# Optimization experiments

Measured on AMD Instinct MI355X. Metric: run time of the kernel, lower is better.

The kernel has to match this reference:

```python
import jax, jax.numpy as jnp
import numpy as np

B, T, PAST, HID = 2, 512, 4096, 4096
HQ, HKV, D = 32, 8, 128
HH_SIZE, RECENT = 512, 512
CACHE = HH_SIZE + RECENT
MAX_POS = PAST + T


def rotate_half(x):
    h = x.shape[-1] // 2
    return jnp.concatenate([-x[..., h:], x[..., :h]], axis=-1)


def setup_inputs() -> dict:
    key = jax.random.key(0)
    ks = jax.random.split(key, 9)
    hidden_states = jax.random.normal(ks[0], (B, T, HID), jnp.float32) * 0.02
    past_k = jax.random.normal(ks[1], (B, HKV, PAST, D), jnp.float32)
    past_v = jax.random.normal(ks[2], (B, HKV, PAST, D), jnp.float32)
    # accumulated heavy-hitter scores are nonnegative attention-mass sums
    hh_prev = jax.random.uniform(ks[3], (B, HKV, PAST), jnp.float32) * float(T)
    wq = jax.random.normal(ks[4], (HID, HQ * D), jnp.float32) * 0.02
    wk = jax.random.normal(ks[5], (HID, HKV * D), jnp.float32) * 0.02
    wv = jax.random.normal(ks[6], (HID, HKV * D), jnp.float32) * 0.02
    wo = jax.random.normal(ks[7], (HQ * D, HID), jnp.float32) * 0.02
    # RoPE tables [1, MAX_POS, D]
    inv_freq = 1.0 / (10000.0 ** (jnp.arange(0, D, 2, dtype=jnp.float32) / D))
    t = jnp.arange(MAX_POS, dtype=jnp.float32)
    freqs = jnp.einsum('t,f->tf', t, inv_freq)
    emb = jnp.concatenate([freqs, freqs], axis=-1)
    cos = jnp.cos(emb)[None]
    sin = jnp.sin(emb)[None]
    position_ids = jnp.broadcast_to(PAST + jnp.arange(T, dtype=jnp.int32)[None, :], (B, T))
    return {"hidden_states": hidden_states, "past_k": past_k, "past_v": past_v,
            "hh_prev": hh_prev, "wq": wq, "wk": wk, "wv": wv, "wo": wo,
            "cos": cos, "sin": sin, "position_ids": position_ids}


def reference(hidden_states, past_k, past_v, hh_prev, wq, wk, wv, wo, cos, sin, position_ids):
    b, t, _ = hidden_states.shape
    # projections -> [B, H, T, D]
    q = (hidden_states @ wq).reshape(b, t, HQ, D).transpose(0, 2, 1, 3)
    k_new = (hidden_states @ wk).reshape(b, t, HKV, D).transpose(0, 2, 1, 3)
    v_new = (hidden_states @ wv).reshape(b, t, HKV, D).transpose(0, 2, 1, 3)
    # RoPE: gather cos/sin at position_ids -> [B, 1, T, D]
    cos_g = cos[0][position_ids][:, None]
    sin_g = sin[0][position_ids][:, None]
    q = q * cos_g + rotate_half(q) * sin_g
    k_new = k_new * cos_g + rotate_half(k_new) * sin_g
    k = jnp.concatenate([past_k, k_new], axis=2)   # [B, HKV, S, D]
    v = jnp.concatenate([past_v, v_new], axis=2)
    s = k.shape[2]
    past_len = s - t
    g = HQ // HKV
    k_rep = jnp.repeat(k, g, axis=1)               # repeat_interleave over heads
    v_rep = jnp.repeat(v, g, axis=1)
    scores = jnp.einsum('bhtd,bhsd->bhts', q, k_rep) / jnp.sqrt(jnp.float32(D))
    causal = jnp.arange(s)[None, :] <= (past_len + jnp.arange(t))[:, None]  # [T, S]
    scores = jnp.where(causal[None, None], scores, jnp.finfo(scores.dtype).min)
    attn = jax.nn.softmax(scores, axis=-1)         # [B, HQ, T, S]
    ctx = jnp.einsum('bhts,bhsd->bhtd', attn, v_rep)
    out = ctx.transpose(0, 2, 1, 3).reshape(b, t, HQ * D) @ wo
    # --- H2O heavy-hitter score update ('average' GQA reduction) ---
    sc = attn.sum(axis=2)                          # [B, HQ, S]
    sc = sc.reshape(b, HKV, g, s).mean(axis=2)     # [B, HKV, S]
    hh = sc.at[:, :, :past_len].add(hh_prev)
    # --- eviction: topk heavy hitters outside recent window + recent window ---
    select = hh[:, :, : s - RECENT]
    _, top = jax.lax.top_k(select, HH_SIZE)
    top = jnp.sort(top, axis=-1)
    recent_idx = jnp.broadcast_to(jnp.arange(s - RECENT, s, dtype=top.dtype), (b, HKV, RECENT))
    keep = jnp.concatenate([top, recent_idx], axis=-1)      # [B, HKV, CACHE]
    k_kept = jnp.take_along_axis(k, keep[..., None], axis=2)
    v_kept = jnp.take_along_axis(v, keep[..., None], axis=2)
    hh_new = jnp.take_along_axis(hh, keep, axis=2)
    return out, k_kept, v_kept, hh_new
```

## Files before the change

### kernel.cpp

```cpp
#include <hip/hip_runtime.h>
#include <cstdint>
#include <cstddef>

typedef unsigned short u16;
typedef __attribute__((ext_vector_type(8))) short short8;
typedef __attribute__((ext_vector_type(4))) float floatx4;

static __device__ __forceinline__ u16 f2bf(float f){
  union { float f; uint32_t i; } u; u.f = f;
  uint32_t i = u.i;
  return (u16)((i + 0x7FFFu + ((i >> 16) & 1u)) >> 16);
}

struct __align__(8) U16x4 { u16 a,b,c,d; };

__global__ void k_convert(const float* __restrict__ src, u16* __restrict__ dst, int n4){
  int i = blockIdx.x*256 + threadIdx.x;
  if (i >= n4) return;
  float4 v = ((const float4*)src)[i];
  U16x4 o{f2bf(v.x), f2bf(v.y), f2bf(v.z), f2bf(v.w)};
  ((U16x4*)dst)[i] = o;
}

__global__ void k_copy_pastk(const float* __restrict__ pk, u16* __restrict__ kcat){
  int i = blockIdx.x*256 + threadIdx.x;
  int slice = i >> 17;
  int off   = i & 131071;
  float4 v = ((const float4*)pk)[i];
  U16x4 o{f2bf(v.x), f2bf(v.y), f2bf(v.z), f2bf(v.w)};
  ((U16x4*)(kcat + (size_t)slice*(4608*128)))[off] = o;
}

__global__ void k_transpose(const float* __restrict__ src, u16* __restrict__ dst,
                            int lds_, int ldd, size_t sstride, size_t dstride){
  src += (size_t)blockIdx.z * sstride; dst += (size_t)blockIdx.z * dstride;
  __shared__ float tile[32][33];
  int bm = blockIdx.y*32, bn = blockIdx.x*32;
  int tx = threadIdx.x & 31, ty = threadIdx.x >> 5;
  #pragma unroll
  for (int r = 0; r < 32; r += 8)
    tile[r+ty][tx] = src[(size_t)(bm + r + ty)*lds_ + bn + tx];
  __syncthreads();
  #pragma unroll
  for (int r = 0; r < 32; r += 8)
    dst[(size_t)(bn + r + ty)*ldd + bm + tx] = f2bf(tile[tx][r+ty]);
}

__global__ __launch_bounds__(256) void k_gemm_bt(
    const u16* __restrict__ A, const u16* __restrict__ Bt, float* __restrict__ C,
    int N, int K)
{
  __shared__ __align__(16) u16 As[128*64];
  __shared__ __align__(16) u16 Bs[128*64];
  const int tid = threadIdx.x, lane = tid & 63, wave = tid >> 6;
  const int m0 = blockIdx.y*128, n0 = blockIdx.x*128;
  const int wr = (wave >> 1)*64, wc = (wave & 1)*64;
  const int srow = tid >> 3, sc8 = tid & 7;
  const u16* ap = A  + (size_t)(m0 + srow)*K + sc8*8;
  const u16* bp = Bt + (size_t)(n0 + srow)*K + sc8*8;
  floatx4 acc[4][4] = {};
  short8 ra[4], rb[4];
  #pragma unroll
  for (int i = 0; i < 4; ++i){
    ra[i] = *(const short8*)(ap + (size_t)i*32*K);
    rb[i] = *(const short8*)(bp + (size_t)i*32*K);
  }
  const int nk = K >> 6;
  for (int kt = 0; kt < nk; ++kt){
    #pragma unroll
    for (int i = 0; i < 4; ++i){
      const int r = srow + i*32;
      const int c = sc8 ^ (r & 7);
      *(short8*)(As + r*64 + c*8) = ra[i];
      *(short8*)(Bs + r*64 + c*8) = rb[i];
    }
    __syncthreads();
    if (kt + 1 < nk){
      const size_t ko = (size_t)(kt+1)*64;
      #pragma unroll
      for (int i = 0; i < 4; ++i){
        ra[i] = *(const short8*)(ap + (size_t)i*32*K + ko);
        rb[i] = *(const short8*)(bp + (size_t)i*32*K + ko);
      }
    }
    #pragma unroll
    for (int ks = 0; ks < 2; ++ks){
      const int c16 = ks*4 + (lane >> 4);
      short8 af[4], bf[4];
      #pragma unroll
      for (int mi = 0; mi < 4; ++mi){
        const int r = wr + mi*16 + (lane & 15);
        af[mi] = *(const short8*)(As + r*64 + ((c16 ^ (r & 7))*8));
      }
      #pragma unroll
      for (int ni = 0; ni < 4; ++ni){
        const int r = wc + ni*16 + (lane & 15);
        bf[ni] = *(const short8*)(Bs + r*64 + ((c16 ^ (r & 7))*8));
      }
      #pragma unroll
      for (int mi = 0; mi < 4; ++mi)
        #pragma unroll
        for (int ni = 0; ni < 4; ++ni)
          acc[mi][ni] = __builtin_amdgcn_mfma_f32_16x16x32_bf16(af[mi], bf[ni], acc[mi][ni], 0,0,0);
    }
    __syncthreads();
  }
  #pragma unroll
  for (int mi = 0; mi < 4; ++mi)
    #pragma unroll
    for (int ni = 0; ni < 4; ++ni){
      const int col = n0 + wc + ni*16 + (lane & 15);
      const int row = m0 + wr + mi*16 + ((lane >> 4) << 2);
      #pragma unroll
      for (int j = 0; j < 4; ++j)
        C[(size_t)(row + j)*N + col] = acc[mi][ni][j];
    }
}

__global__ void k_rope_q(const float* __restrict__ qf, const float* __restrict__ cosb,
                         const float* __restrict__ sinb, const int* __restrict__ pid,
                         u16* __restrict__ qbo){
  int gid = blockIdx.x*256 + threadIdx.x;
  int d = gid & 63, hh = (gid >> 6) & 31, m = gid >> 11;
  int b = m >> 9, t = m & 511;
  int p = pid[b*512 + t];
  float c = cosb[(size_t)p*128 + d], s = sinb[(size_t)p*128 + d];
  size_t ib = (size_t)m*4096 + hh*128 + d;
  float x = qf[ib], y = qf[ib + 64];
  const float sc = 0.08838834764831845f;
  size_t ob = (((size_t)(b*32 + hh))*512 + t)*128 + d;
  qbo[ob]      = f2bf((x*c - y*s)*sc);
  qbo[ob + 64] = f2bf((y*c + x*s)*sc);
}

__global__ void k_rope_kv(const float* __restrict__ kvf, const float* __restrict__ cosb,
                          const float* __restrict__ sinb, const int* __restrict__ pid,
                          u16* __restrict__ kcat, float* __restrict__ knr, u16* __restrict__ vtcat){
  int gid = blockIdx.x*256 + threadIdx.x;
  int d = gid & 63, kv = (gid >> 6) & 7, m = gid >> 9;
  int b = m >> 9, t = m & 511;
  int p = pid[b*512 + t];
  float c = cosb[(size_t)p*128 + d], s = sinb[(size_t)p*128 + d];
  size_t ib = (size_t)m*2048 + kv*128 + d;
  float x = kvf[ib], y = kvf[ib + 64];
  float k0 = x*c - y*s, k1 = y*c + x*s;
  int bk = b*8 + kv;
  size_t kb = ((size_t)bk*4608 + 4096 + t)*128 + d;
  kcat[kb] = f2bf(k0); kcat[kb + 64] = f2bf(k1);
  size_t nb = ((size_t)bk*512 + t)*128 + d;
  knr[nb] = k0; knr[nb + 64] = k1;
  float v0 = kvf[ib + 1024], v1 = kvf[ib + 1088];
  size_t vb = (size_t)bk*(128*4608) + (size_t)d*4608 + 4096 + t;
  vtcat[vb] = f2bf(v0);
  vtcat[vb + (size_t)64*4608] = f2bf(v1);
}

__global__ __launch_bounds__(256) void k_attn(
    const u16* __restrict__ qb, const u16* __restrict__ kcat,
    const u16* __restrict__ vtcat, u16* __restrict__ ctxb,
    float* __restrict__ part_sc)
{
  __shared__ __align__(16) u16 kvlds[64*128];
  __shared__ __align__(16) float plds[64*68];
  __shared__ float cs[4608];

  const int tid = threadIdx.x, lane = tid & 63, wave = tid >> 6;
  const int bid = blockIdx.x;
  const int slice  = (bid & 7) + 8*((bid >> 3) >> 5);
  const int within = (bid >> 3) & 31;
  const int b  = slice >> 3;
  const int kv = slice & 7;
  const int h  = kv*4 + (within >> 3);
  const int tb = within & 7;
  const int t0 = tb * 64;

  const u16* qp = qb + (((size_t)(b*32 + h))*512 + t0) * 128;
  const u16* kp = kcat  + (size_t)slice * (4608*128);
  const u16* vp = vtcat + (size_t)slice * (128*4608);

  for (int i = tid; i < 4608; i += 256) cs[i] = 0.f;

  short8 qf[4];
  {
    const int r = wave*16 + (lane & 15);
    const u16* q0 = qp + (size_t)r*128 + ((lane>>4)*8);
    #pragma unroll
    for (int ks = 0; ks < 4; ++ks) qf[ks] = *(const short8*)(q0 + ks*32);
  }

  const int ntiles = 65 + tb;
  float l0=0.f, l1=0.f, l2=0.f, l3=0.f;

  for (int st = 0; st < ntiles; ++st){
    const int s0 = st * 64;
    __syncthreads();
    {
      const int c16 = tid & 15;
      #pragma unroll
      for (int i = 0; i < 4; ++i){
        const int row = i*16 + (tid >> 4);
        short8 v = *(const short8*)(kp + (size_t)(s0 + row)*128 + c16*8);
        *(short8*)(kvlds + row*128 + ((c16 ^ (row & 7))*8)) = v;
      }
    }
    __syncthreads();
    floatx4 sacc[4] = {};
    #pragma unroll
    for (int ks = 0; ks < 4; ++ks){
      const int c16 = ks*4 + (lane >> 4);
      #pragma unroll
      for (int nf = 0; nf < 4; ++nf){
        const int r = nf*16 + (lane & 15);
        short8 kf = *(const short8*)(kvlds + r*128 + ((c16 ^ (r & 7))*8));
        sacc[nf] = __builtin_amdgcn_mfma_f32_16x16x32_bf16(qf[ks], kf, sacc[nf], 0,0,0);
      }
    }
    const bool lastt = (st == ntiles-1);
    #pragma unroll
    for (int nf = 0; nf < 4; ++nf){
      #pragma unroll
      for (int j = 0; j < 4; ++j){
        float e = __expf(sacc[nf][j]);
        if (lastt){
          int scol = nf*16 + (lane & 15);
          int tloc = wave*16 + ((lane >> 4) << 2) + j;
          if (scol > tloc) e = 0.f;
        }
        if (j==0) l0 += e; else if (j==1) l1 += e; else if (j==2) l2 += e; else l3 += e;
      }
    }
  }
  #pragma unroll
  for (int m = 1; m <= 8; m <<= 1){
    l0 += __shfl_xor(l0, m); l1 += __shfl_xor(l1, m);
    l2 += __shfl_xor(l2, m); l3 += __shfl_xor(l3, m);
  }
  const float rl0 = 1.f/l0, rl1 = 1.f/l1, rl2 = 1.f/l2, rl3 = 1.f/l3;

  floatx4 pacc[8] = {};
  const int prow = wave*16 + (lane & 15);
  for (int st = 0; st < ntiles; ++st){
    const int s0 = st*64;
    __syncthreads();
    {
      const int c16 = tid & 15;
      #pragma unroll
      for (int i = 0; i < 4; ++i){
        const int row = i*16 + (tid >> 4);
        short8 v = *(const short8*)(kp + (size_t)(s0 + row)*128 + c16*8);
        *(short8*)(kvlds + row*128 + ((c16 ^ (row & 7))*8)) = v;
      }
    }
    __syncthreads();
    floatx4 sacc[4] = {};
    #pragma unroll
    for (int ks = 0; ks < 4; ++ks){
      const int c16 = ks*4 + (lane >> 4);
      #pragma unroll
      for (int nf = 0; nf < 4; ++nf){
        const int r = nf*16 + (lane & 15);
        short8 kf = *(const short8*)(kvlds + r*128 + ((c16 ^ (r & 7))*8));
        sacc[nf] = __builtin_amdgcn_mfma_f32_16x16x32_bf16(qf[ks], kf, sacc[nf], 0,0,0);
      }
    }
    const bool lastt = (st == ntiles-1);
    float cs0=0.f, cs1=0.f, cs2=0.f, cs3=0.f;
    #pragma unroll
    for (int nf = 0; nf < 4; ++nf){
      float cpart = 0.f;
      #pragma unroll
      for (int j = 0; j < 4; ++j){
        float e = __expf(sacc[nf][j]);
        if (lastt){
          int scol = nf*16 + (lane & 15);
          int tloc = wave*16 + ((lane >> 4) << 2) + j;
          if (scol > tloc) e = 0.f;
        }
        float rl = (j==0)?rl0:(j==1)?rl1:(j==2)?rl2:rl3;
        float p = e * rl;
        plds[(wave*16 + ((lane>>4)<<2) + j)*68 + nf*16 + (lane & 15)] = p;
        cpart += p;
      }
      if (nf==0) cs0=cpart; else if (nf==1) cs1=cpart; else if (nf==2) cs2=cpart; else cs3=cpart;
    }
    cs0 += __shfl_xor(cs0,16); cs0 += __shfl_xor(cs0,32);
    cs1 += __shfl_xor(cs1,16); cs1 += __shfl_xor(cs1,32);
    cs2 += __shfl_xor(cs2,16); cs2 += __shfl_xor(cs2,32);
    cs3 += __shfl_xor(cs3,16); cs3 += __shfl_xor(cs3,32);
    {
      const int nfsel = lane >> 4;
      float v = (nfsel==0)?cs0:(nfsel==1)?cs1:(nfsel==2)?cs2:cs3;
      atomicAdd(&cs[s0 + nfsel*16 + (lane & 15)], v);
    }
    __syncthreads();
    {
      const int c = tid & 7;
      #pragma unroll
      for (int i = 0; i < 4; ++i){
        const int row = i*32 + (tid >> 3);
        short8 v = *(const short8*)(vp + (size_t)row*4608 + s0 + c*8);
        *(short8*)(kvlds + row*64 + ((c ^ (row & 7))*8)) = v;
      }
    }
    __syncthreads();
    short8 pa[2];
    #pragma unroll
    for (int k2 = 0; k2 < 2; ++k2){
      const int sbase = k2*32 + ((lane>>4)*8);
      const float* pp = plds + prow*68 + sbase;
      float4 x = *(const float4*)pp;
      float4 y = *(const float4*)(pp + 4);
      short8 t8;
      t8[0]=(short)f2bf(x.x); t8[1]=(short)f2bf(x.y); t8[2]=(short)f2bf(x.z); t8[3]=(short)f2bf(x.w);
      t8[4]=(short)f2bf(y.x); t8[5]=(short)f2bf(y.y); t8[6]=(short)f2bf(y.z); t8[7]=(short)f2bf(y.w);
      pa[k2] = t8;
    }
    #pragma unroll
    for (int nf = 0; nf < 8; ++nf){
      const int rv = nf*16 + (lane & 15);
      #pragma unroll
      for (int k2 = 0; k2 < 2; ++k2){
        const int c = ((k2*4 + (lane>>4)) ^ (rv & 7));
        short8 vf = *(const short8*)(kvlds + rv*64 + c*8);
        pacc[nf] = __builtin_amdgcn_mfma_f32_16x16x32_bf16(pa[k2], vf, pacc[nf], 0,0,0);
      }
    }
  }
  #pragma unroll
  for (int nf = 0; nf < 8; ++nf)
    #pragma unroll
    for (int j = 0; j < 4; ++j){
      const int trow = t0 + wave*16 + ((lane>>4)<<2) + j;
      const int col  = h*128 + nf*16 + (lane & 15);
      ctxb[(size_t)(b*512 + trow)*4096 + col] = f2bf(pacc[nf][j]);
    }
  __syncthreads();
  {
    float* pr = part_sc + (((size_t)(b*32 + h))*8 + tb)*4608;
    for (int i = tid; i < 4608; i += 256) pr[i] = cs[i];
  }
}

__global__ void k_hh_reduce(const float* __restrict__ part, const float* __restrict__ hhprev,
                            float* __restrict__ hh){
  int gid = blockIdx.x*256 + threadIdx.x;
  if (gid >= 73728) return;
  int s = gid % 4608; int bk = gid / 4608; int b = bk >> 3, kv = bk & 7;
  float acc = 0.f;
  #pragma unroll
  for (int h4 = 0; h4 < 4; ++h4){
    const float* pp = part + (((size_t)(b*32 + kv*4 + h4))*8)*4608 + s;
    #pragma unroll
    for (int tbb = 0; tbb < 8; ++tbb) acc += pp[(size_t)tbb*4608];
  }
  acc *= 0.25f;
  if (s < 4096) acc += hhprev[(size_t)bk*4096 + s];
  hh[gid] = acc;
}

__global__ __launch_bounds__(256) void k_topk(const float* __restrict__ hh, int* __restrict__ keep,
                                              float* __restrict__ hh_new){
  __shared__ uint64_t keys[4096];
  __shared__ int sidx[512];
  const int bk = blockIdx.x, tid = threadIdx.x;
  const float* hp = hh + (size_t)bk*4608;
  for (int i = tid; i < 4096; i += 256){
    uint32_t vb = __float_as_uint(hp[i]);
    keys[i] = ((uint64_t)(0xFFFFFFFFu - vb) << 12) | (uint32_t)i;
  }
  __syncthreads();
  for (int k = 2; k <= 4096; k <<= 1){
    for (int j = k >> 1; j > 0; j >>= 1){
      for (int i = tid; i < 4096; i += 256){
        int ixj = i ^ j;
        if (ixj > i){
          uint64_t a = keys[i], c = keys[ixj];
          bool up = ((i & k) == 0);
          if ((a > c) == up){ keys[i] = c; keys[ixj] = a; }
        }
      }
      __syncthreads();
    }
  }
  for (int i = tid; i < 512; i += 256) sidx[i] = (int)(keys[i] & 0xFFF);
  __syncthreads();
  for (int k = 2; k <= 512; k <<= 1){
    for (int j = k >> 1; j > 0; j >>= 1){
      for (int i = tid; i < 512; i += 256){
        int ixj = i ^ j;
        if (ixj > i){
          int a = sidx[i], c = sidx[ixj];
          bool up = ((i & k) == 0);
          if ((a > c) == up){ sidx[i] = c; sidx[ixj] = a; }
        }
      }
      __syncthreads();
    }
  }
  for (int i = tid; i < 512; i += 256){
    int id = sidx[i];
    keep[bk*1024 + i] = id;
    hh_new[(size_t)bk*1024 + i] = hp[id];
    keep[bk*1024 + 512 + i] = 4096 + i;
    hh_new[(size_t)bk*1024 + 512 + i] = hp[4096 + i];
  }
}

__global__ void k_gather(const float* __restrict__ pastk, const float* __restrict__ pastv,
                         const float* __restrict__ knr, const float* __restrict__ kvf,
                         const int* __restrict__ keep,
                         float* __restrict__ outk, float* __restrict__ outv){
  int r = blockIdx.x*2 + (threadIdx.x >> 7);
  int lane = threadIdx.x & 127;
  int bk = r >> 10, i = r & 1023;
  int idx = keep[bk*1024 + i];
  float kval, vval;
  if (idx < 4096){
    kval = pastk[((size_t)bk*4096 + idx)*128 + lane];
    vval = pastv[((size_t)bk*4096 + idx)*128 + lane];
  } else {
    int t = idx - 4096; int b = bk >> 3, kv = bk & 7;
    kval = knr[((size_t)bk*512 + t)*128 + lane];
    vval = kvf[(size_t)(b*512 + t)*2048 + 1024 + kv*128 + lane];
  }
  outk[(size_t)r*128 + lane] = kval;
  outv[(size_t)r*128 + lane] = vval;
}

extern "C" void kernel_launch(void* const* d_in, const int* in_sizes, int n_in,
                              void* d_out, int out_size, void* d_ws, size_t ws_size,
                              hipStream_t stream){
  const float* hs     = (const float*)d_in[0];
  const float* pastk  = (const float*)d_in[1];
  const float* pastv  = (const float*)d_in[2];
  const float* hhprev = (const float*)d_in[3];
  const float* wq     = (const float*)d_in[4];
  const float* wk     = (const float*)d_in[5];
  const float* wv     = (const float*)d_in[6];
  const float* wo     = (const float*)d_in[7];
  const float* cosb   = (const float*)d_in[8];
  const float* sinb   = (const float*)d_in[9];
  const int*   pid    = (const int*)d_in[10];
  float* out = (float*)d_out;
  char* ws = (char*)d_ws;

  u16*   hsb  = (u16*)(ws + 0);
  u16*   wqt  = (u16*)(ws + 8388608);
  u16*   wkvt = (u16*)(ws + 41943040);
  float* qf   = (float*)(ws + 58720256);
  float* part = qf;
  float* kvf  = (float*)(ws + 75497472);
  u16*   qb   = (u16*)(ws + 83886080);
  u16*   kcat = (u16*)(ws + 92274688);
  u16*   vtc  = (u16*)(ws + 111149056);
  float* knr  = (float*)(ws + 130023424);
  u16*   ctxb = (u16*)(ws + 138412032);
  float* hhb  = (float*)(ws + 146800640);
  int*   keep = (int*)(ws + 147095552);

  (void)in_sizes; (void)n_in; (void)out_size; (void)ws_size;

  k_convert<<<4096,256,0,stream>>>(hs, hsb, 1048576);
  k_transpose<<<dim3(128,128,1),256,0,stream>>>(wq, wqt, 4096, 4096, 0, 0);
  k_transpose<<<dim3(32,128,1),256,0,stream>>>(wk, wkvt, 1024, 4096, 0, 0);
  k_transpose<<<dim3(32,128,1),256,0,stream>>>(wv, wkvt + (size_t)1024*4096, 1024, 4096, 0, 0);
  k_transpose<<<dim3(4,128,16),256,0,stream>>>(pastv, vtc, 128, 4608,
                                               (size_t)4096*128, (size_t)128*4608);
  k_copy_pastk<<<8192,256,0,stream>>>(pastk, kcat);

  k_gemm_bt<<<dim3(32,8),256,0,stream>>>(hsb, wqt, qf, 4096, 4096);
  k_gemm_bt<<<dim3(16,8),256,0,stream>>>(hsb, wkvt, kvf, 2048, 4096);
  k_transpose<<<dim3(128,128,1),256,0,stream>>>(wo, wqt, 4096, 4096, 0, 0);

  k_rope_q<<<8192,256,0,stream>>>(qf, cosb, sinb, pid, qb);
  k_rope_kv<<<2048,256,0,stream>>>(kvf, cosb, sinb, pid, kcat, knr, vtc);

  k_attn<<<512,256,0,stream>>>(qb, kcat, vtc, ctxb, part);

  k_gemm_bt<<<dim3(32,8),256,0,stream>>>(ctxb, wqt, out, 4096, 4096);

  k_hh_reduce<<<288,256,0,stream>>>(part, hhprev, hhb);
  k_topk<<<16,256,0,stream>>>(hhb, keep, out + 8388608);
  k_gather<<<8192,256,0,stream>>>(pastk, pastv, knr, kvf, keep,
                                  out + 4194304, out + 6291456);
}
```

Before: 906.5 us.

## Split-K GEMMs and split attention into parallel row-sum and PV passes

Adds split-K (two K halves written to separate buffers) to the projection and output GEMMs, so each launches twice as many blocks; the halves are summed in the rope kernels and a new add kernel. Attention is split into a row-sum-of-exp pass over 2048 blocks, each covering a chunk of key tiles, followed by a PV pass with register-prefetched K and V tiles loaded together. Column sums go to a per-wave LDS buffer and are written directly instead of through shared atomics. The gather recomputes RoPE for new keys instead of storing a float copy. The cost is more memory traffic for partial buffers and an extra QK pass.

Result: faster. 789.3 us (-12.9%).

```diff
diff --git a/kernel.cpp b/kernel.cpp
--- a/kernel.cpp
+++ b/kernel.cpp
@@ -48,24 +48,26 @@
 
 __global__ __launch_bounds__(256) void k_gemm_bt(
     const u16* __restrict__ A, const u16* __restrict__ Bt, float* __restrict__ C,
-    int N, int K)
+    int N, int Kfull, int kLen, size_t cstride)
 {
   __shared__ __align__(16) u16 As[128*64];
   __shared__ __align__(16) u16 Bs[128*64];
   const int tid = threadIdx.x, lane = tid & 63, wave = tid >> 6;
   const int m0 = blockIdx.y*128, n0 = blockIdx.x*128;
+  const int kOff = blockIdx.z * kLen;
+  C += (size_t)blockIdx.z * cstride;
   const int wr = (wave >> 1)*64, wc = (wave & 1)*64;
   const int srow = tid >> 3, sc8 = tid & 7;
-  const u16* ap = A  + (size_t)(m0 + srow)*K + sc8*8;
-  const u16* bp = Bt + (size_t)(n0 + srow)*K + sc8*8;
+  const u16* ap = A  + (size_t)(m0 + srow)*Kfull + kOff + sc8*8;
+  const u16* bp = Bt + (size_t)(n0 + srow)*Kfull + kOff + sc8*8;
   floatx4 acc[4][4] = {};
   short8 ra[4], rb[4];
   #pragma unroll
   for (int i = 0; i < 4; ++i){
-    ra[i] = *(const short8*)(ap + (size_t)i*32*K);
-    rb[i] = *(const short8*)(bp + (size_t)i*32*K);
-  }
-  const int nk = K >> 6;
+    ra[i] = *(const short8*)(ap + (size_t)i*32*Kfull);
+    rb[i] = *(const short8*)(bp + (size_t)i*32*Kfull);
+  }
+  const int nk = kLen >> 6;
   for (int kt = 0; kt < nk; ++kt){
     #pragma unroll
     for (int i = 0; i < 4; ++i){
@@ -79,8 +81,8 @@
       const size_t ko = (size_t)(kt+1)*64;
       #pragma unroll
       for (int i = 0; i < 4; ++i){
-        ra[i] = *(const short8*)(ap + (size_t)i*32*K + ko);
-        rb[i] = *(const short8*)(bp + (size_t)i*32*K + ko);
+        ra[i] = *(const short8*)(ap + (size_t)i*32*Kfull + ko);
+        rb[i] = *(const short8*)(bp + (size_t)i*32*Kfull + ko);
       }
     }
     #pragma unroll
@@ -117,171 +119,238 @@
     }
 }
 
-__global__ void k_rope_q(const float* __restrict__ qf, const float* __restrict__ cosb,
-                         const float* __restrict__ sinb, const int* __restrict__ pid,
-                         u16* __restrict__ qbo){
+__global__ void k_add(const float* __restrict__ a, const float* __restrict__ b,
+                      float* __restrict__ o, int n4){
+  int i = blockIdx.x*256 + threadIdx.x;
+  if (i >= n4) return;
+  float4 x = ((const float4*)a)[i], y = ((const float4*)b)[i];
+  float4 z; z.x=x.x+y.x; z.y=x.y+y.y; z.z=x.z+y.z; z.w=x.w+y.w;
+  ((float4*)o)[i] = z;
+}
+
+__global__ void k_rope_q(const float* __restrict__ qfA, const float* __restrict__ qfB,
+                         const float* __restrict__ cosb, const float* __restrict__ sinb,
+                         const int* __restrict__ pid, u16* __restrict__ qbo){
   int gid = blockIdx.x*256 + threadIdx.x;
   int d = gid & 63, hh = (gid >> 6) & 31, m = gid >> 11;
   int b = m >> 9, t = m & 511;
   int p = pid[b*512 + t];
   float c = cosb[(size_t)p*128 + d], s = sinb[(size_t)p*128 + d];
   size_t ib = (size_t)m*4096 + hh*128 + d;
-  float x = qf[ib], y = qf[ib + 64];
+  float x = qfA[ib] + qfB[ib], y = qfA[ib+64] + qfB[ib+64];
   const float sc = 0.08838834764831845f;
   size_t ob = (((size_t)(b*32 + hh))*512 + t)*128 + d;
   qbo[ob]      = f2bf((x*c - y*s)*sc);
   qbo[ob + 64] = f2bf((y*c + x*s)*sc);
 }
 
-__global__ void k_rope_kv(const float* __restrict__ kvf, const float* __restrict__ cosb,
-                          const float* __restrict__ sinb, const int* __restrict__ pid,
-                          u16* __restrict__ kcat, float* __restrict__ knr, u16* __restrict__ vtcat){
+__global__ void k_rope_kv(const float* __restrict__ kvfA, const float* __restrict__ kvfB,
+                          const float* __restrict__ cosb, const float* __restrict__ sinb,
+                          const int* __restrict__ pid,
+                          u16* __restrict__ kcat, u16* __restrict__ vtcat){
   int gid = blockIdx.x*256 + threadIdx.x;
   int d = gid & 63, kv = (gid >> 6) & 7, m = gid >> 9;
   int b = m >> 9, t = m & 511;
   int p = pid[b*512 + t];
   float c = cosb[(size_t)p*128 + d], s = sinb[(size_t)p*128 + d];
   size_t ib = (size_t)m*2048 + kv*128 + d;
-  float x = kvf[ib], y = kvf[ib + 64];
+  float x = kvfA[ib] + kvfB[ib], y = kvfA[ib+64] + kvfB[ib+64];
   float k0 = x*c - y*s, k1 = y*c + x*s;
   int bk = b*8 + kv;
   size_t kb = ((size_t)bk*4608 + 4096 + t)*128 + d;
   kcat[kb] = f2bf(k0); kcat[kb + 64] = f2bf(k1);
-  size_t nb = ((size_t)bk*512 + t)*128 + d;
-  knr[nb] = k0; knr[nb + 64] = k1;
-  float v0 = kvf[ib + 1024], v1 = kvf[ib + 1088];
+  float v0 = kvfA[ib+1024] + kvfB[ib+1024];
+  float v1 = kvfA[ib+1088] + kvfB[ib+1088];
   size_t vb = (size_t)bk*(128*4608) + (size_t)d*4608 + 4096 + t;
   vtcat[vb] = f2bf(v0);
   vtcat[vb + (size_t)64*4608] = f2bf(v1);
 }
 
-__global__ __launch_bounds__(256) void k_attn(
+__global__ __launch_bounds__(256) void k_attn_l(
     const u16* __restrict__ qb, const u16* __restrict__ kcat,
-    const u16* __restrict__ vtcat, u16* __restrict__ ctxb,
-    float* __restrict__ part_sc)
+    float* __restrict__ lpart)
 {
-  __shared__ __align__(16) u16 kvlds[64*128];
-  __shared__ __align__(16) float plds[64*68];
-  __shared__ float cs[4608];
-
+  __shared__ __align__(16) u16 kl[64*128];
   const int tid = threadIdx.x, lane = tid & 63, wave = tid >> 6;
   const int bid = blockIdx.x;
-  const int slice  = (bid & 7) + 8*((bid >> 3) >> 5);
-  const int within = (bid >> 3) & 31;
-  const int b  = slice >> 3;
-  const int kv = slice & 7;
-  const int h  = kv*4 + (within >> 3);
-  const int tb = within & 7;
-  const int t0 = tb * 64;
-
-  const u16* qp = qb + (((size_t)(b*32 + h))*512 + t0) * 128;
-  const u16* kp = kcat  + (size_t)slice * (4608*128);
-  const u16* vp = vtcat + (size_t)slice * (128*4608);
-
-  for (int i = tid; i < 4608; i += 256) cs[i] = 0.f;
+  const int slice = (bid & 7) + 8*(bid >> 10);
+  const int within = (bid >> 3) & 127;
+  const int b = slice >> 3, kv = slice & 7;
+  const int h = kv*4 + (within >> 5);
+  const int tb = (within >> 2) & 7;
+  const int sc = within & 3;
+  const int t0 = tb*64;
+  const int ntiles = 65 + tb;
+  const int st0 = sc*18;
+  const int st1 = (st0 + 18 < ntiles) ? (st0 + 18) : ntiles;
+  const u16* qp = qb + (((size_t)(b*32+h))*512 + t0)*128;
+  const u16* kp = kcat + (size_t)slice*(4608*128);
 
   short8 qf[4];
   {
     const int r = wave*16 + (lane & 15);
     const u16* q0 = qp + (size_t)r*128 + ((lane>>4)*8);
     #pragma unroll
-    for (int ks = 0; ks < 4; ++ks) qf[ks] = *(const short8*)(q0 + ks*32);
-  }
-
-  const int ntiles = 65 + tb;
-  float l0=0.f, l1=0.f, l2=0.f, l3=0.f;
-
-  for (int st = 0; st < ntiles; ++st){
-    const int s0 = st * 64;
+    for (int ks=0; ks<4; ++ks) qf[ks] = *(const short8*)(q0 + ks*32);
+  }
+  const int c16 = tid & 15, srow = tid >> 4;
+  short8 rk[4];
+  #pragma unroll
+  for (int i=0;i<4;++i)
+    rk[i] = *(const short8*)(kp + (size_t)(st0*64 + i*16 + srow)*128 + c16*8);
+
+  float l0=0.f,l1=0.f,l2=0.f,l3=0.f;
+  for (int st=st0; st<st1; ++st){
     __syncthreads();
-    {
-      const int c16 = tid & 15;
-      #pragma unroll
-      for (int i = 0; i < 4; ++i){
-        const int row = i*16 + (tid >> 4);
-        short8 v = *(const short8*)(kp + (size_t)(s0 + row)*128 + c16*8);
-        *(short8*)(kvlds + row*128 + ((c16 ^ (row & 7))*8)) = v;
-      }
+    #pragma unroll
+    for (int i=0;i<4;++i){
+      const int row = i*16 + srow;
+      *(short8*)(kl + row*128 + ((c16 ^ (row&7))*8)) = rk[i];
     }
     __syncthreads();
+    if (st+1 < st1){
+      #pragma unroll
+      for (int i=0;i<4;++i)
+        rk[i] = *(const short8*)(kp + (size_t)((st+1)*64 + i*16 + srow)*128 + c16*8);
+    }
     floatx4 sacc[4] = {};
     #pragma unroll
-    for (int ks = 0; ks < 4; ++ks){
-      const int c16 = ks*4 + (lane >> 4);
-      #pragma unroll
-      for (int nf = 0; nf < 4; ++nf){
-        const int r = nf*16 + (lane & 15);
-        short8 kf = *(const short8*)(kvlds + r*128 + ((c16 ^ (r & 7))*8));
+    for (int ks=0; ks<4; ++ks){
+      const int cc = ks*4 + (lane>>4);
+      #pragma unroll
+      for (int nf=0; nf<4; ++nf){
+        const int r = nf*16 + (lane&15);
+        short8 kf = *(const short8*)(kl + r*128 + ((cc ^ (r&7))*8));
         sacc[nf] = __builtin_amdgcn_mfma_f32_16x16x32_bf16(qf[ks], kf, sacc[nf], 0,0,0);
       }
     }
     const bool lastt = (st == ntiles-1);
     #pragma unroll
-    for (int nf = 0; nf < 4; ++nf){
-      #pragma unroll
-      for (int j = 0; j < 4; ++j){
+    for (int nf=0;nf<4;++nf)
+      #pragma unroll
+      for (int j=0;j<4;++j){
         float e = __expf(sacc[nf][j]);
         if (lastt){
-          int scol = nf*16 + (lane & 15);
-          int tloc = wave*16 + ((lane >> 4) << 2) + j;
+          int scol = nf*16 + (lane&15);
+          int tloc = wave*16 + ((lane>>4)<<2) + j;
           if (scol > tloc) e = 0.f;
         }
-        if (j==0) l0 += e; else if (j==1) l1 += e; else if (j==2) l2 += e; else l3 += e;
-      }
-    }
-  }
-  #pragma unroll
-  for (int m = 1; m <= 8; m <<= 1){
-    l0 += __shfl_xor(l0, m); l1 += __shfl_xor(l1, m);
-    l2 += __shfl_xor(l2, m); l3 += __shfl_xor(l3, m);
-  }
-  const float rl0 = 1.f/l0, rl1 = 1.f/l1, rl2 = 1.f/l2, rl3 = 1.f/l3;
-
+        if(j==0)l0+=e; else if(j==1)l1+=e; else if(j==2)l2+=e; else l3+=e;
+      }
+  }
+  #pragma unroll
+  for (int m=1; m<=8; m<<=1){
+    l0 += __shfl_xor(l0,m); l1 += __shfl_xor(l1,m);
+    l2 += __shfl_xor(l2,m); l3 += __shfl_xor(l3,m);
+  }
+  if ((lane & 15) == 0){
+    float* lp = lpart + ((((size_t)(b*32+h))*8 + tb)<<8) + (sc<<6) + wave*16 + ((lane>>4)<<2);
+    lp[0]=l0; lp[1]=l1; lp[2]=l2; lp[3]=l3;
+  }
+}
+
+__global__ __launch_bounds__(256) void k_attn_pv(
+    const u16* __restrict__ qb, const u16* __restrict__ kcat,
+    const u16* __restrict__ vtcat, const float* __restrict__ lpart,
+    u16* __restrict__ ctxb, float* __restrict__ part)
+{
+  __shared__ __align__(16) u16 kl[64*128];
+  __shared__ __align__(16) u16 vl[128*64];
+  __shared__ __align__(16) float plds[64*68];
+  __shared__ float cw[4*64];
+
+  const int tid=threadIdx.x, lane=tid&63, wave=tid>>6;
+  const int bid=blockIdx.x;
+  const int slice = (bid&7) + 8*((bid>>3)>>5);
+  const int within = (bid>>3)&31;
+  const int b=slice>>3, kv=slice&7;
+  const int h = kv*4 + (within>>3);
+  const int tb = within&7;
+  const int t0 = tb*64;
+  const int ntiles = 65+tb;
+  const u16* qp = qb + (((size_t)(b*32+h))*512 + t0)*128;
+  const u16* kp = kcat + (size_t)slice*(4608*128);
+  const u16* vp = vtcat + (size_t)slice*(128*4608);
+  float* pb = part + (((size_t)(b*32+h))*8 + tb)*4608;
+
+  float rl[4];
+  {
+    const float* lp = lpart + ((((size_t)(b*32+h))*8 + tb)<<8);
+    const int r0 = wave*16 + ((lane>>4)<<2);
+    #pragma unroll
+    for (int j=0;j<4;++j){
+      int r = r0 + j;
+      float l = lp[r] + lp[64+r] + lp[128+r] + lp[192+r];
+      rl[j] = 1.f/l;
+    }
+  }
+  short8 qf[4];
+  {
+    const int r = wave*16 + (lane & 15);
+    const u16* q0 = qp + (size_t)r*128 + ((lane>>4)*8);
+    #pragma unroll
+    for (int ks=0; ks<4; ++ks) qf[ks] = *(const short8*)(q0 + ks*32);
+  }
+  const int c16 = tid&15, srow = tid>>4;
+  const int vc = tid&7,  vrow = tid>>3;
+  short8 rk[4], rv[4];
+  #pragma unroll
+  for (int i=0;i<4;++i){
+    rk[i] = *(const short8*)(kp + (size_t)(i*16 + srow)*128 + c16*8);
+    rv[i] = *(const short8*)(vp + (size_t)(i*32 + vrow)*4608 + vc*8);
+  }
   floatx4 pacc[8] = {};
-  const int prow = wave*16 + (lane & 15);
-  for (int st = 0; st < ntiles; ++st){
+  const int prow = wave*16 + (lane&15);
+
+  for (int st=0; st<ntiles; ++st){
     const int s0 = st*64;
     __syncthreads();
-    {
-      const int c16 = tid & 15;
-      #pragma unroll
-      for (int i = 0; i < 4; ++i){
-        const int row = i*16 + (tid >> 4);
-        short8 v = *(const short8*)(kp + (size_t)(s0 + row)*128 + c16*8);
-        *(short8*)(kvlds + row*128 + ((c16 ^ (row & 7))*8)) = v;
-      }
+    if (st > 0 && tid < 64)
+      pb[s0-64+tid] = cw[tid] + cw[64+tid] + cw[128+tid] + cw[192+tid];
+    #pragma unroll
+    for (int i=0;i<4;++i){
+      const int row = i*16 + srow;
+      *(short8*)(kl + row*128 + ((c16 ^ (row&7))*8)) = rk[i];
+      const int vr = i*32 + vrow;
+      *(short8*)(vl + vr*64 + ((vc ^ (vr&7))*8)) = rv[i];
     }
     __syncthreads();
+    if (st+1 < ntiles){
+      #pragma unroll
+      for (int i=0;i<4;++i){
+        rk[i] = *(const short8*)(kp + (size_t)((st+1)*64 + i*16 + srow)*128 + c16*8);
+        rv[i] = *(const short8*)(vp + (size_t)(i*32 + vrow)*4608 + (st+1)*64 + vc*8);
+      }
+    }
     floatx4 sacc[4] = {};
     #pragma unroll
-    for (int ks = 0; ks < 4; ++ks){
-      const int c16 = ks*4 + (lane >> 4);
-      #pragma unroll
-      for (int nf = 0; nf < 4; ++nf){
-        const int r = nf*16 + (lane & 15);
-        short8 kf = *(const short8*)(kvlds + r*128 + ((c16 ^ (r & 7))*8));
+    for (int ks=0; ks<4; ++ks){
+      const int cc = ks*4 + (lane>>4);
+      #pragma unroll
+      for (int nf=0; nf<4; ++nf){
+        const int r = nf*16 + (lane&15);
+        short8 kf = *(const short8*)(kl + r*128 + ((cc ^ (r&7))*8));
         sacc[nf] = __builtin_amdgcn_mfma_f32_16x16x32_bf16(qf[ks], kf, sacc[nf], 0,0,0);
       }
     }
-    const bool lastt = (st == ntiles-1);
+    const bool lastt = (st==ntiles-1);
     float cs0=0.f, cs1=0.f, cs2=0.f, cs3=0.f;
     #pragma unroll
-    for (int nf = 0; nf < 4; ++nf){
-      float cpart = 0.f;
-      #pragma unroll
-      for (int j = 0; j < 4; ++j){
+    for (int nf=0;nf<4;++nf){
+      float cpart=0.f;
+      #pragma unroll
+      for (int j=0;j<4;++j){
         float e = __expf(sacc[nf][j]);
         if (lastt){
-          int scol = nf*16 + (lane & 15);
-          int tloc = wave*16 + ((lane >> 4) << 2) + j;
+          int scol = nf*16 + (lane&15);
+          int tloc = wave*16 + ((lane>>4)<<2) + j;
           if (scol > tloc) e = 0.f;
         }
-        float rl = (j==0)?rl0:(j==1)?rl1:(j==2)?rl2:rl3;
-        float p = e * rl;
-        plds[(wave*16 + ((lane>>4)<<2) + j)*68 + nf*16 + (lane & 15)] = p;
+        float p = e * rl[j];
+        plds[(wave*16 + ((lane>>4)<<2) + j)*68 + nf*16 + (lane&15)] = p;
         cpart += p;
       }
-      if (nf==0) cs0=cpart; else if (nf==1) cs1=cpart; else if (nf==2) cs2=cpart; else cs3=cpart;
+      if(nf==0)cs0=cpart; else if(nf==1)cs1=cpart; else if(nf==2)cs2=cpart; else cs3=cpart;
     }
     cs0 += __shfl_xor(cs0,16); cs0 += __shfl_xor(cs0,32);
     cs1 += __shfl_xor(cs1,16); cs1 += __shfl_xor(cs1,32);
@@ -290,19 +359,8 @@
     {
       const int nfsel = lane >> 4;
       float v = (nfsel==0)?cs0:(nfsel==1)?cs1:(nfsel==2)?cs2:cs3;
-      atomicAdd(&cs[s0 + nfsel*16 + (lane & 15)], v);
-    }
-    __syncthreads();
-    {
-      const int c = tid & 7;
-      #pragma unroll
-      for (int i = 0; i < 4; ++i){
-        const int row = i*32 + (tid >> 3);
-        short8 v = *(const short8*)(vp + (size_t)row*4608 + s0 + c*8);
-        *(short8*)(kvlds + row*64 + ((c ^ (row & 7))*8)) = v;
-      }
-    }
-    __syncthreads();
+      cw[wave*64 + nfsel*16 + (lane & 15)] = v;
+    }
     short8 pa[2];
     #pragma unroll
     for (int k2 = 0; k2 < 2; ++k2){
@@ -317,15 +375,18 @@
     }
     #pragma unroll
     for (int nf = 0; nf < 8; ++nf){
-      const int rv = nf*16 + (lane & 15);
+      const int rv2 = nf*16 + (lane & 15);
       #pragma unroll
       for (int k2 = 0; k2 < 2; ++k2){
-        const int c = ((k2*4 + (lane>>4)) ^ (rv & 7));
-        short8 vf = *(const short8*)(kvlds + rv*64 + c*8);
+        const int c = ((k2*4 + (lane>>4)) ^ (rv2 & 7));
+        short8 vf = *(const short8*)(vl + rv2*64 + c*8);
         pacc[nf] = __builtin_amdgcn_mfma_f32_16x16x32_bf16(pa[k2], vf, pacc[nf], 0,0,0);
       }
     }
   }
+  __syncthreads();
+  if (tid < 64)
+    pb[(ntiles-1)*64 + tid] = cw[tid] + cw[64+tid] + cw[128+tid] + cw[192+tid];
   #pragma unroll
   for (int nf = 0; nf < 8; ++nf)
     #pragma unroll
@@ -334,11 +395,6 @@
       const int col  = h*128 + nf*16 + (lane & 15);
       ctxb[(size_t)(b*512 + trow)*4096 + col] = f2bf(pacc[nf][j]);
     }
-  __syncthreads();
-  {
-    float* pr = part_sc + (((size_t)(b*32 + h))*8 + tb)*4608;
-    for (int i = tid; i < 4608; i += 256) pr[i] = cs[i];
-  }
 }
 
 __global__ void k_hh_reduce(const float* __restrict__ part, const float* __restrict__ hhprev,
@@ -351,7 +407,8 @@
   for (int h4 = 0; h4 < 4; ++h4){
     const float* pp = part + (((size_t)(b*32 + kv*4 + h4))*8)*4608 + s;
     #pragma unroll
-    for (int tbb = 0; tbb < 8; ++tbb) acc += pp[(size_t)tbb*4608];
+    for (int tbb = 0; tbb < 8; ++tbb)
+      if (s < 4160 + tbb*64) acc += pp[(size_t)tbb*4608];
   }
   acc *= 0.25f;
   if (s < 4096) acc += hhprev[(size_t)bk*4096 + s];
@@ -407,24 +464,31 @@
 }
 
 __global__ void k_gather(const float* __restrict__ pastk, const float* __restrict__ pastv,
-                         const float* __restrict__ knr, const float* __restrict__ kvf,
-                         const int* __restrict__ keep,
+                         const float* __restrict__ kvfA, const float* __restrict__ kvfB,
+                         const float* __restrict__ cosb, const float* __restrict__ sinb,
+                         const int* __restrict__ pid, const int* __restrict__ keep,
                          float* __restrict__ outk, float* __restrict__ outv){
   int r = blockIdx.x*2 + (threadIdx.x >> 7);
-  int lane = threadIdx.x & 127;
+  int d = threadIdx.x & 127;
   int bk = r >> 10, i = r & 1023;
   int idx = keep[bk*1024 + i];
   float kval, vval;
   if (idx < 4096){
-    kval = pastk[((size_t)bk*4096 + idx)*128 + lane];
-    vval = pastv[((size_t)bk*4096 + idx)*128 + lane];
+    kval = pastk[((size_t)bk*4096 + idx)*128 + d];
+    vval = pastv[((size_t)bk*4096 + idx)*128 + d];
   } else {
     int t = idx - 4096; int b = bk >> 3, kv = bk & 7;
-    kval = knr[((size_t)bk*512 + t)*128 + lane];
-    vval = kvf[(size_t)(b*512 + t)*2048 + 1024 + kv*128 + lane];
-  }
-  outk[(size_t)r*128 + lane] = kval;
-  outv[(size_t)r*128 + lane] = vval;
+    size_t base = ((size_t)(b*512 + t))*2048 + kv*128;
+    int dp = (d < 64) ? d + 64 : d - 64;
+    float x  = kvfA[base + d]  + kvfB[base + d];
+    float xp = kvfA[base + dp] + kvfB[base + dp];
+    int p = pid[b*512 + t];
+    float c = cosb[(size_t)p*128 + d], s = sinb[(size_t)p*128 + d];
+    kval = x*c + xp*((d < 64) ? -s : s);
+    vval = kvfA[base + 1024 + d] + kvfB[base + 1024 + d];
+  }
+  outk[(size_t)r*128 + d] = kval;
+  outv[(size_t)r*128 + d] = vval;
 }
 
 extern "C" void kernel_launch(void* const* d_in, const int* in_sizes, int n_in,
@@ -447,16 +511,18 @@
   u16*   hsb  = (u16*)(ws + 0);
   u16*   wqt  = (u16*)(ws + 8388608);
   u16*   wkvt = (u16*)(ws + 41943040);
-  float* qf   = (float*)(ws + 58720256);
-  float* part = qf;
-  float* kvf  = (float*)(ws + 75497472);
-  u16*   qb   = (u16*)(ws + 83886080);
-  u16*   kcat = (u16*)(ws + 92274688);
-  u16*   vtc  = (u16*)(ws + 111149056);
-  float* knr  = (float*)(ws + 130023424);
-  u16*   ctxb = (u16*)(ws + 138412032);
-  float* hhb  = (float*)(ws + 146800640);
-  int*   keep = (int*)(ws + 147095552);
+  float* qfA  = (float*)(ws + 58720256);
+  float* qfB  = (float*)(ws + 75497472);
+  float* kvfA = (float*)(ws + 92274688);
+  float* kvfB = (float*)(ws + 100663296);
+  u16*   qb   = (u16*)(ws + 109051904);
+  u16*   kcat = (u16*)(ws + 117440512);
+  u16*   vtc  = (u16*)(ws + 136314880);
+  u16*   ctxb = (u16*)(ws + 155189248);
+  float* part = (float*)(ws + 163577856);
+  float* lprt = (float*)(ws + 173015040);
+  float* hhb  = (float*)(ws + 173539328);
+  int*   keep = (int*)(ws + 173834240);
 
   (void)in_sizes; (void)n_in; (void)out_size; (void)ws_size;
 
@@ -468,19 +534,21 @@
                                                (size_t)4096*128, (size_t)128*4608);
   k_copy_pastk<<<8192,256,0,stream>>>(pastk, kcat);
 
-  k_gemm_bt<<<dim3(32,8),256,0,stream>>>(hsb, wqt, qf, 4096, 4096);
-  k_gemm_bt<<<dim3(16,8),256,0,stream>>>(hsb, wkvt, kvf, 2048, 4096);
+  k_gemm_bt<<<dim3(32,8,2),256,0,stream>>>(hsb, wqt, qfA, 4096, 4096, 2048, (size_t)1024*4096);
+  k_gemm_bt<<<dim3(16,8,2),256,0,stream>>>(hsb, wkvt, kvfA, 2048, 4096, 2048, (size_t)1024*2048);
   k_transpose<<<dim3(128,128,1),256,0,stream>>>(wo, wqt, 4096, 4096, 0, 0);
 
-  k_rope_q<<<8192,256,0,stream>>>(qf, cosb, sinb, pid, qb);
-  k_rope_kv<<<2048,256,0,stream>>>(kvf, cosb, sinb, pid, kcat, knr, vtc);
-
-  k_attn<<<512,256,0,stream>>>(qb, kcat, vtc, ctxb, part);
-
-  k_gemm_bt<<<dim3(32,8),256,0,stream>>>(ctxb, wqt, out, 4096, 4096);
+  k_rope_q<<<8192,256,0,stream>>>(qfA, qfB, cosb, sinb, pid, qb);
+  k_rope_kv<<<2048,256,0,stream>>>(kvfA, kvfB, cosb, sinb, pid, kcat, vtc);
+
+  k_attn_l<<<2048,256,0,stream>>>(qb, kcat, lprt);
+  k_attn_pv<<<512,256,0,stream>>>(qb, kcat, vtc, lprt, ctxb, part);
+
+  k_gemm_bt<<<dim3(32,8,2),256,0,stream>>>(ctxb, wqt, qfA, 4096, 4096, 2048, (size_t)1024*4096);
+  k_add<<<4096,256,0,stream>>>(qfA, qfB, out, 1048576);
 
   k_hh_reduce<<<288,256,0,stream>>>(part, hhprev, hhb);
   k_topk<<<16,256,0,stream>>>(hhb, keep, out + 8388608);
-  k_gather<<<8192,256,0,stream>>>(pastk, pastv, knr, kvf, keep,
+  k_gather<<<8192,256,0,stream>>>(pastk, pastv, kvfA, kvfB, cosb, sinb, pid, keep,
                                   out + 4194304, out + 6291456);
 }
```
